# Kernel tuning notes

Hardware: AMD Instinct MI355X
Metric: run time of the kernel (lower is better)

Reference implementation:

```python
import jax, jax.numpy as jnp
import numpy as np


def _conv2d(x, w, b):
    # x: [B,C,H,W], w: [O,I,kh,kw] (SAME padding, stride 1)
    y = jax.lax.conv_general_dilated(x, w, (1, 1), 'SAME',
                                     dimension_numbers=('NCHW', 'OIHW', 'NCHW'))
    return y + b[None, :, None, None]


def _conv1x1(x, w, b):
    # w: [O,C], b: [O]
    return jnp.einsum('oc,bchw->bohw', w, x) + b[None, :, None, None]


def _attention(xq, xkv, w, b):
    # w: [3,C,C] (q,k,v), b: [3,C]. Tokens = spatial positions, features = channels.
    B, C, H, W = xq.shape
    q = _conv1x1(xq, w[0], b[0]).reshape(B, C, H * W).transpose(0, 2, 1)   # [B,HW,C]
    k = _conv1x1(xkv, w[1], b[1]).reshape(B, C, H * W).transpose(0, 2, 1)
    v = _conv1x1(xkv, w[2], b[2]).reshape(B, C, H * W).transpose(0, 2, 1)
    scale = 1.0 / jnp.sqrt(jnp.asarray(C, xq.dtype))  # d_k = channels
    a = jax.nn.softmax(jnp.einsum('bnc,bmc->bnm', q, k) * scale, axis=-1)  # [B,HW,HW]
    out = jnp.einsum('bnm,bmc->bnc', a, v).transpose(0, 2, 1).reshape(B, C, H, W)
    return out + xq


def _cell(x, h, c, w, b):
    gates = _conv2d(jnp.concatenate([x, h], axis=1), w, b)
    i, f, o, g = jnp.split(gates, 4, axis=1)
    i, f, o, g = jax.nn.sigmoid(i), jax.nn.sigmoid(f), jax.nn.sigmoid(o), jnp.tanh(g)
    c_new = f * c + i * g
    h_new = o * jnp.tanh(c_new)
    return h_new, c_new


def setup_inputs() -> dict:
    key = jax.random.key(0)
    ks = iter(jax.random.split(key, 32))
    B, T, Cin, H, W = 2, 3, 1, 32, 32
    HID, L, K, OUT = 64, 2, 3, 1
    s = 0.02
    d = {
        'x1_seq': jax.random.normal(next(ks), (B, T, Cin, H, W), jnp.float32),
        'x2_seq': jax.random.normal(next(ks), (B, T, Cin, H, W), jnp.float32),
        # ConvLSTM gate convs: layer0 in = Cin+HID, layer1 in = 2*HID, per stream
        'conv1_w0': jax.random.normal(next(ks), (4 * HID, Cin + HID, K, K)) * s,
        'conv1_b0': jnp.zeros((4 * HID,)),
        'conv1_w1': jax.random.normal(next(ks), (4 * HID, 2 * HID, K, K)) * s,
        'conv1_b1': jnp.zeros((4 * HID,)),
        'conv2_w0': jax.random.normal(next(ks), (4 * HID, Cin + HID, K, K)) * s,
        'conv2_b0': jnp.zeros((4 * HID,)),
        'conv2_w1': jax.random.normal(next(ks), (4 * HID, 2 * HID, K, K)) * s,
        'conv2_b1': jnp.zeros((4 * HID,)),
        # attention 1x1 convs, stacked [L, 3(q/k/v), HID, HID]
        'sah_w': jax.random.normal(next(ks), (L, 3, HID, HID)) * s,
        'sah_b': jnp.zeros((L, 3, HID)),
        'sac_w': jax.random.normal(next(ks), (L, 3, HID, HID)) * s,
        'sac_b': jnp.zeros((L, 3, HID)),
        'cah_w': jax.random.normal(next(ks), (L, 3, HID, HID)) * s,
        'cah_b': jnp.zeros((L, 3, HID)),
        'cac_w': jax.random.normal(next(ks), (L, 3, HID, HID)) * s,
        'cac_b': jnp.zeros((L, 3, HID)),
        # decoder
        'dec_w1': jax.random.normal(next(ks), (HID, HID, 3, 3)) * s,
        'dec_b1': jnp.zeros((HID,)),
        'dec_w2': jax.random.normal(next(ks), (OUT, HID, 3, 3)) * s,
        'dec_b2': jnp.zeros((OUT,)),
        'future_steps': 4,
    }
    return d


def reference(x1_seq, x2_seq,
              conv1_w0, conv1_b0, conv1_w1, conv1_b1,
              conv2_w0, conv2_b0, conv2_w1, conv2_b1,
              sah_w, sah_b, sac_w, sac_b, cah_w, cah_b, cac_w, cac_b,
              dec_w1, dec_b1, dec_w2, dec_b2, future_steps):
    B, T, _, H, W = x1_seq.shape
    HID = sah_w.shape[-1]
    L = sah_w.shape[0]
    cw1 = [(conv1_w0, conv1_b0), (conv1_w1, conv1_b1)]
    cw2 = [(conv2_w0, conv2_b0), (conv2_w1, conv2_b1)]

    def decoder(h):
        return _conv2d(jax.nn.relu(_conv2d(h, dec_w1, dec_b1)), dec_w2, dec_b2)

    z = jnp.zeros((B, HID, H, W), x1_seq.dtype)
    h1s, c1s = [z] * L, [z] * L
    h2s, c2s = [z] * L, [z] * L

    def step(x1_t, x2_t, h1s, c1s, h2s, c2s):
        h1s, c1s, h2s, c2s = list(h1s), list(c1s), list(h2s), list(c2s)
        for l in range(L):
            h1, c1 = _cell(x1_t, h1s[l], c1s[l], *cw1[l])
            h2, c2 = _cell(x2_t, h2s[l], c2s[l], *cw2[l])
            h1 = _attention(h1, h1, sah_w[l], sah_b[l])
            c1 = _attention(c1, c1, sac_w[l], sac_b[l])
            h2 = _attention(h2, h2, sah_w[l], sah_b[l])
            c2 = _attention(c2, c2, sac_w[l], sac_b[l])
            tag_h1, tag_c1 = h1, c1
            h1 = _attention(h1, h2, cah_w[l], cah_b[l])
            c1 = _attention(c1, c2, cac_w[l], cac_b[l])
            h2 = _attention(h2, tag_h1, cah_w[l], cah_b[l])
            c2 = _attention(c2, tag_c1, cac_w[l], cac_b[l])
            h1s[l], c1s[l], h2s[l], c2s[l] = h1, c1, h2, c2
            x1_t, x2_t = h1, h2
        return h1s, c1s, h2s, c2s

    warm1, warm2 = [], []
    for t in range(T):
        h1s, c1s, h2s, c2s = step(x1_seq[:, t], x2_seq[:, t], h1s, c1s, h2s, c2s)
        if t < T - 1:
            warm1.append(h1s[-1])
            warm2.append(h2s[-1])
    pred_warm1 = jnp.stack([decoder(h) for h in warm1], axis=1)
    pred_warm2 = jnp.stack([decoder(h) for h in warm2], axis=1)

    preds1, preds2 = [], []
    for _ in range(int(future_steps)):
        p1 = decoder(h1s[-1])
        p2 = decoder(h2s[-1])
        preds1.append(p1)
        preds2.append(p2)
        h1s, c1s, h2s, c2s = step(p1, p2, h1s, c1s, h2s, c2s)
    preds1 = jnp.stack(preds1, axis=1)
    preds2 = jnp.stack(preds2, axis=1)
    return preds1, preds2, pred_warm1, pred_warm2
```

## Files before the change

kernel.cpp:

```cpp
#include <hip/hip_runtime.h>
#include <math.h>

#define BB 2
#define HIDC 64
#define HWN 1024

struct CellArgs {
  const float* x[2]; long xbs;
  const float* h[2]; const float* c[2];
  const float* w[2]; const float* bias[2];
  float* ho[2]; float* co[2];
};

template<int CX>
__global__ __launch_bounds__(512) void cell_kernel(CellArgs a) {
  constexpr int CT = CX + HIDC;
  constexpr int CH = (CT + 1) / 2;
  __shared__ float sIn[CT * 48];
  __shared__ float sGa[256 * 17];
  __shared__ float sGb[256 * 17];
  const int tile = blockIdx.x;
  const int b = blockIdx.y;
  const int st = blockIdx.z;
  const int ty0 = (tile >> 3) << 2, tx0 = (tile & 7) << 2;
  const float* xp = a.x[st] + (size_t)b * a.xbs;
  const float* hp = a.h[st] + (size_t)b * HIDC * HWN;

  for (int idx = threadIdx.x; idx < CT * 36; idx += 512) {
    int ic = idx / 36, pos = idx - ic * 36;
    int iy = pos / 6, ix = pos - iy * 6;
    int gy = ty0 - 1 + iy, gx = tx0 - 1 + ix;
    float v = 0.f;
    if ((unsigned)gy < 32u && (unsigned)gx < 32u) {
      v = (ic < CX) ? xp[ic * HWN + gy * 32 + gx]
                    : hp[(ic - CX) * HWN + gy * 32 + gx];
    }
    sIn[ic * 48 + iy * 8 + ix] = v;
  }
  __syncthreads();

  const int oc = threadIdx.x & 255;
  const int hh = threadIdx.x >> 8;
  const int icb = hh ? CH : 0, ice = hh ? CT : CH;
  float acc[16];
#pragma unroll
  for (int p = 0; p < 16; ++p) acc[p] = 0.f;
  const float* wp = a.w[st] + (size_t)oc * CT * 9;
  for (int ic = icb; ic < ice; ++ic) {
    float w9[9];
#pragma unroll
    for (int t = 0; t < 9; ++t) w9[t] = wp[ic * 9 + t];
    float in[36];
#pragma unroll
    for (int iy = 0; iy < 6; ++iy) {
      float4 v4 = *(const float4*)&sIn[ic * 48 + iy * 8];
      float2 v2 = *(const float2*)&sIn[ic * 48 + iy * 8 + 4];
      in[iy * 6 + 0] = v4.x; in[iy * 6 + 1] = v4.y; in[iy * 6 + 2] = v4.z;
      in[iy * 6 + 3] = v4.w; in[iy * 6 + 4] = v2.x; in[iy * 6 + 5] = v2.y;
    }
#pragma unroll
    for (int ky = 0; ky < 3; ++ky)
#pragma unroll
      for (int kx = 0; kx < 3; ++kx) {
        const float wv = w9[ky * 3 + kx];
#pragma unroll
        for (int py = 0; py < 4; ++py)
#pragma unroll
          for (int px = 0; px < 4; ++px)
            acc[py * 4 + px] += wv * in[(py + ky) * 6 + (px + kx)];
      }
  }
  float* sGh = hh ? sGb : sGa;
#pragma unroll
  for (int p = 0; p < 16; ++p) sGh[oc * 17 + p] = acc[p];
  __syncthreads();

  const float* cp = a.c[st] + (size_t)b * HIDC * HWN;
  float* hop = a.ho[st] + (size_t)b * HIDC * HWN;
  float* cop = a.co[st] + (size_t)b * HIDC * HWN;
  const float* bias = a.bias[st];
  for (int idx = threadIdx.x; idx < HIDC * 16; idx += 512) {
    int hc = idx >> 4, p = idx & 15;
    float gi = sGa[hc * 17 + p]         + sGb[hc * 17 + p]         + bias[hc];
    float gf = sGa[(hc + 64) * 17 + p]  + sGb[(hc + 64) * 17 + p]  + bias[hc + 64];
    float go = sGa[(hc + 128) * 17 + p] + sGb[(hc + 128) * 17 + p] + bias[hc + 128];
    float gg = sGa[(hc + 192) * 17 + p] + sGb[(hc + 192) * 17 + p] + bias[hc + 192];
    gi = 1.f / (1.f + expf(-gi));
    gf = 1.f / (1.f + expf(-gf));
    go = 1.f / (1.f + expf(-go));
    gg = tanhf(gg);
    int off = hc * HWN + (ty0 + (p >> 2)) * 32 + tx0 + (p & 3);
    float cn = gf * cp[off] + gi * gg;
    cop[off] = cn;
    hop[off] = go * tanhf(cn);
  }
}

struct QkvArgs {
  const float* xq[4]; const float* xkv[4];
  const float* w[4]; const float* bias[4];
  float* Q; float* K; float* V;
};

__global__ __launch_bounds__(256) void qkv_kernel(QkvArgs a) {
  __shared__ float sWt[64 * 68];
  const int ptile = blockIdx.x, b = blockIdx.y;
  const int attn = blockIdx.z / 3, proj = blockIdx.z % 3;
  const float* x = (proj == 0 ? a.xq[attn] : a.xkv[attn]) + (size_t)b * HIDC * HWN;
  const float* w = a.w[attn] + proj * 64 * 64;
  const float* bias = a.bias[attn] + proj * 64;
  float* dst = (proj == 0 ? a.Q : (proj == 1 ? a.K : a.V)) +
               ((size_t)attn * BB + b) * HWN * HIDC;
  for (int i = threadIdx.x; i < 4096; i += 256) {
    int o = i >> 6, c = i & 63;
    sWt[c * 68 + o] = w[i];
  }
  __syncthreads();
  const int og = threadIdx.x & 3, pq = threadIdx.x >> 2;
  const int p0 = ptile * 128 + pq * 2;
  float acc[2][16];
#pragma unroll
  for (int k = 0; k < 16; ++k) {
    float bv = bias[og * 16 + k];
    acc[0][k] = bv; acc[1][k] = bv;
  }
  for (int c = 0; c < 64; ++c) {
    float2 xv = *(const float2*)&x[c * HWN + p0];
#pragma unroll
    for (int k = 0; k < 16; k += 4) {
      float4 wv = *(const float4*)&sWt[c * 68 + og * 16 + k];
      acc[0][k+0] += xv.x*wv.x; acc[0][k+1] += xv.x*wv.y; acc[0][k+2] += xv.x*wv.z; acc[0][k+3] += xv.x*wv.w;
      acc[1][k+0] += xv.y*wv.x; acc[1][k+1] += xv.y*wv.y; acc[1][k+2] += xv.y*wv.z; acc[1][k+3] += xv.y*wv.w;
    }
  }
#pragma unroll
  for (int px = 0; px < 2; ++px) {
    float* d = dst + (size_t)(p0 + px) * HIDC + og * 16;
#pragma unroll
    for (int k = 0; k < 16; k += 4) {
      float4 v; v.x = acc[px][k]; v.y = acc[px][k+1]; v.z = acc[px][k+2]; v.w = acc[px][k+3];
      *(float4*)&d[k] = v;
    }
  }
}

struct AttnPArgs { const float* Q; const float* K; const float* V; float* pbuf; };

__global__ __launch_bounds__(256) void attn_part(AttnPArgs a) {
  __shared__ float sQt[64 * 36];
  __shared__ float sKt[64 * 68];
  __shared__ float sV [64 * 68];
  __shared__ float sPt[64 * 36];
  const int qt = blockIdx.x >> 2, ks = blockIdx.x & 3;
  const int b = blockIdx.y, at = blockIdx.z;
  const size_t base = ((size_t)at * BB + b) * HWN * HIDC;
  const float* Qp = a.Q + base + (size_t)qt * 32 * HIDC;
  const float* Kp = a.K + base;
  const float* Vp = a.V + base;
  const int tid = threadIdx.x;
  {
    int r = tid >> 3, c0 = (tid & 7) * 8;
    const float* q = Qp + r * HIDC + c0;
#pragma unroll
    for (int k = 0; k < 8; k += 4) {
      float4 v = *(const float4*)&q[k];
      sQt[(c0 + k + 0) * 36 + r] = v.x * 0.125f;
      sQt[(c0 + k + 1) * 36 + r] = v.y * 0.125f;
      sQt[(c0 + k + 2) * 36 + r] = v.z * 0.125f;
      sQt[(c0 + k + 3) * 36 + r] = v.w * 0.125f;
    }
  }
  const int tc = tid & 15, tr = tid >> 4;
  const int r0 = tr * 2, j0 = tc * 4;
  const int kj = tid & 63, kch = (tid >> 6) * 16;
  const int sj = tid >> 2, scs = (tid & 3) * 16;
  float m0 = -1e30f, m1 = -1e30f, l0 = 0.f, l1 = 0.f;
  float o00=0,o01=0,o02=0,o03=0,o10=0,o11=0,o12=0,o13=0;

  const int ktb = ks * 4;
  float4 kr[4], vr[4];
  {
    const float* kp = Kp + (size_t)(ktb * 64 + kj) * HIDC + kch;
    const float* vp = Vp + (size_t)(ktb * 64 + sj) * HIDC + scs;
#pragma unroll
    for (int q = 0; q < 4; ++q) {
      kr[q] = *(const float4*)&kp[q * 4];
      vr[q] = *(const float4*)&vp[q * 4];
    }
  }

  for (int kk = 0; kk < 4; ++kk) {
    __syncthreads();
#pragma unroll
    for (int q = 0; q < 4; ++q) {
      sKt[(kch + q * 4 + 0) * 68 + kj] = kr[q].x;
      sKt[(kch + q * 4 + 1) * 68 + kj] = kr[q].y;
      sKt[(kch + q * 4 + 2) * 68 + kj] = kr[q].z;
      sKt[(kch + q * 4 + 3) * 68 + kj] = kr[q].w;
      *(float4*)&sV[sj * 68 + scs + q * 4] = vr[q];
    }
    __syncthreads();
    if (kk < 3) {
      const float* kp = Kp + (size_t)((ktb + kk + 1) * 64 + kj) * HIDC + kch;
      const float* vp = Vp + (size_t)((ktb + kk + 1) * 64 + sj) * HIDC + scs;
#pragma unroll
      for (int q = 0; q < 4; ++q) {
        kr[q] = *(const float4*)&kp[q * 4];
        vr[q] = *(const float4*)&vp[q * 4];
      }
    }
    float s00=0,s01=0,s02=0,s03=0,s10=0,s11=0,s12=0,s13=0;
#pragma unroll 4
    for (int c = 0; c < 64; ++c) {
      float2 qv = *(const float2*)&sQt[c * 36 + r0];
      float4 kv = *(const float4*)&sKt[c * 68 + j0];
      s00 += qv.x*kv.x; s01 += qv.x*kv.y; s02 += qv.x*kv.z; s03 += qv.x*kv.w;
      s10 += qv.y*kv.x; s11 += qv.y*kv.y; s12 += qv.y*kv.z; s13 += qv.y*kv.w;
    }
    float mt0 = fmaxf(fmaxf(s00, s01), fmaxf(s02, s03));
    float mt1 = fmaxf(fmaxf(s10, s11), fmaxf(s12, s13));
#pragma unroll
    for (int d = 1; d < 16; d <<= 1) {
      mt0 = fmaxf(mt0, __shfl_xor(mt0, d));
      mt1 = fmaxf(mt1, __shfl_xor(mt1, d));
    }
    float mn0 = fmaxf(m0, mt0), mn1 = fmaxf(m1, mt1);
    float al0 = __expf(m0 - mn0), al1 = __expf(m1 - mn1);
    s00 = __expf(s00 - mn0); s01 = __expf(s01 - mn0);
    s02 = __expf(s02 - mn0); s03 = __expf(s03 - mn0);
    s10 = __expf(s10 - mn1); s11 = __expf(s11 - mn1);
    s12 = __expf(s12 - mn1); s13 = __expf(s13 - mn1);
    float ps0 = s00 + s01 + s02 + s03, ps1 = s10 + s11 + s12 + s13;
#pragma unroll
    for (int d = 1; d < 16; d <<= 1) {
      ps0 += __shfl_xor(ps0, d);
      ps1 += __shfl_xor(ps1, d);
    }
    l0 = l0 * al0 + ps0; l1 = l1 * al1 + ps1;
    m0 = mn0; m1 = mn1;
    o00*=al0; o01*=al0; o02*=al0; o03*=al0;
    o10*=al1; o11*=al1; o12*=al1; o13*=al1;
    float2 pv;
    pv.x=s00; pv.y=s10; *(float2*)&sPt[(j0+0)*36 + r0] = pv;
    pv.x=s01; pv.y=s11; *(float2*)&sPt[(j0+1)*36 + r0] = pv;
    pv.x=s02; pv.y=s12; *(float2*)&sPt[(j0+2)*36 + r0] = pv;
    pv.x=s03; pv.y=s13; *(float2*)&sPt[(j0+3)*36 + r0] = pv;
    __syncthreads();
#pragma unroll 4
    for (int j = 0; j < 64; ++j) {
      float2 pj = *(const float2*)&sPt[j * 36 + r0];
      float4 vv = *(const float4*)&sV[j * 68 + j0];
      o00 += pj.x*vv.x; o01 += pj.x*vv.y; o02 += pj.x*vv.z; o03 += pj.x*vv.w;
      o10 += pj.y*vv.x; o11 += pj.y*vv.y; o12 += pj.y*vv.z; o13 += pj.y*vv.w;
    }
  }
  float* pb = a.pbuf + ((((size_t)at * BB + b) * 32 + qt) * 4 + ks) * 2112;
  float4 w0; w0.x=o00; w0.y=o01; w0.z=o02; w0.w=o03;
  float4 w1; w1.x=o10; w1.y=o11; w1.z=o12; w1.w=o13;
  *(float4*)&pb[r0 * 64 + j0] = w0;
  *(float4*)&pb[(r0 + 1) * 64 + j0] = w1;
  if (tc == 0) {
    pb[2048 + r0] = m0; pb[2048 + r0 + 1] = m1;
    pb[2080 + r0] = l0; pb[2080 + r0 + 1] = l1;
  }
}

struct AttnMArgs { const float* pbuf; const float* xq[4]; float* out[4]; };

__global__ __launch_bounds__(256) void attn_merge(AttnMArgs a) {
  const int qt = blockIdx.x, b = blockIdx.y, at = blockIdx.z;
  const float* pb = a.pbuf + (((size_t)at * BB + b) * 32 + qt) * 4 * 2112;
  const int c = threadIdx.x >> 2;
  const int rq = (threadIdx.x & 3) * 8;
  const float* xq = a.xq[at] + (size_t)b * HIDC * HWN;
  float* op = a.out[at] + (size_t)b * HIDC * HWN;
  const int p0 = qt * 32 + rq;
  float res[8];
#pragma unroll
  for (int rr = 0; rr < 8; ++rr) {
    int r = rq + rr;
    float mm0 = pb[2048 + r],            mm1 = pb[2112 + 2048 + r];
    float mm2 = pb[2*2112 + 2048 + r],   mm3 = pb[3*2112 + 2048 + r];
    float M = fmaxf(fmaxf(mm0, mm1), fmaxf(mm2, mm3));
    float w0 = __expf(mm0 - M), w1 = __expf(mm1 - M);
    float w2 = __expf(mm2 - M), w3 = __expf(mm3 - M);
    float L = pb[2080 + r]*w0 + pb[2112 + 2080 + r]*w1 +
              pb[2*2112 + 2080 + r]*w2 + pb[3*2112 + 2080 + r]*w3;
    float acc = pb[r*64 + c]*w0 + pb[2112 + r*64 + c]*w1 +
                pb[2*2112 + r*64 + c]*w2 + pb[3*2112 + r*64 + c]*w3;
    res[rr] = acc / L;
  }
  float4 x0 = *(const float4*)&xq[(size_t)c * HWN + p0];
  float4 x1 = *(const float4*)&xq[(size_t)c * HWN + p0 + 4];
  float4 o0, o1;
  o0.x = res[0] + x0.x; o0.y = res[1] + x0.y; o0.z = res[2] + x0.z; o0.w = res[3] + x0.w;
  o1.x = res[4] + x1.x; o1.y = res[5] + x1.y; o1.z = res[6] + x1.z; o1.w = res[7] + x1.w;
  *(float4*)&op[(size_t)c * HWN + p0] = o0;
  *(float4*)&op[(size_t)c * HWN + p0 + 4] = o1;
}

struct Dec1Args { const float* in[2]; const float* w; const float* b; float* tmp; };

__global__ __launch_bounds__(512) void dec1_kernel(Dec1Args a) {
  __shared__ float sIn[64 * 48];
  __shared__ float sHa[64 * 17];
  __shared__ float sHb[64 * 17];
  const int tile = blockIdx.x, b = blockIdx.y, st = blockIdx.z;
  const int ty0 = (tile >> 3) << 2, tx0 = (tile & 7) << 2;
  const float* ip = a.in[st] + (size_t)b * HIDC * HWN;
  for (int idx = threadIdx.x; idx < 64 * 36; idx += 512) {
    int ic = idx / 36, pos = idx - ic * 36;
    int iy = pos / 6, ix = pos - iy * 6;
    int gy = ty0 - 1 + iy, gx = tx0 - 1 + ix;
    float v = 0.f;
    if ((unsigned)gy < 32u && (unsigned)gx < 32u) v = ip[ic * HWN + gy * 32 + gx];
    sIn[ic * 48 + iy * 8 + ix] = v;
  }
  __syncthreads();
  const int oc = threadIdx.x & 63, ps = (threadIdx.x >> 6) & 3;
  const int hh = threadIdx.x >> 8;
  const int icb = hh * 32, ice = icb + 32;
  float acc0 = 0.f, acc1 = 0.f, acc2 = 0.f, acc3 = 0.f;
  const float* wp = a.w + (size_t)oc * 64 * 9;
  for (int ic = icb; ic < ice; ++ic) {
    float in[18];
#pragma unroll
    for (int ry = 0; ry < 3; ++ry) {
      float4 v4 = *(const float4*)&sIn[ic * 48 + (ps + ry) * 8];
      float2 v2 = *(const float2*)&sIn[ic * 48 + (ps + ry) * 8 + 4];
      in[ry*6+0]=v4.x; in[ry*6+1]=v4.y; in[ry*6+2]=v4.z; in[ry*6+3]=v4.w;
      in[ry*6+4]=v2.x; in[ry*6+5]=v2.y;
    }
#pragma unroll
    for (int ky = 0; ky < 3; ++ky)
#pragma unroll
      for (int kx = 0; kx < 3; ++kx) {
        float wv = wp[ic * 9 + ky * 3 + kx];
        acc0 += wv * in[ky * 6 + kx + 0];
        acc1 += wv * in[ky * 6 + kx + 1];
        acc2 += wv * in[ky * 6 + kx + 2];
        acc3 += wv * in[ky * 6 + kx + 3];
      }
  }
  float* sH = hh ? sHb : sHa;
  sH[oc * 17 + ps * 4 + 0] = acc0;
  sH[oc * 17 + ps * 4 + 1] = acc1;
  sH[oc * 17 + ps * 4 + 2] = acc2;
  sH[oc * 17 + ps * 4 + 3] = acc3;
  __syncthreads();
  float* dst = a.tmp + ((size_t)st * BB + b) * HIDC * HWN;
  for (int idx = threadIdx.x; idx < 1024; idx += 512) {
    int oc2 = idx >> 4, p = idx & 15;
    float v = sHa[oc2 * 17 + p] + sHb[oc2 * 17 + p] + a.b[oc2];
    v = fmaxf(v, 0.f);
    dst[(size_t)oc2 * HWN + (ty0 + (p >> 2)) * 32 + tx0 + (p & 3)] = v;
  }
}

struct Dec2Args { const float* tmp; const float* w; const float* b;
                  float* dst0; float* dst1; long bstr; };

__global__ __launch_bounds__(256) void dec2_kernel(Dec2Args a) {
  __shared__ float sIn[64 * 48];
  __shared__ float sW[64 * 9];
  const int tile = blockIdx.x, b = blockIdx.y, st = blockIdx.z;
  const int ty0 = (tile >> 3) << 2, tx0 = (tile & 7) << 2;
  const float* ip = a.tmp + ((size_t)st * BB + b) * HIDC * HWN;
  for (int idx = threadIdx.x; idx < 64 * 36; idx += 256) {
    int ic = idx / 36, pos = idx - ic * 36;
    int iy = pos / 6, ix = pos - iy * 6;
    int gy = ty0 - 1 + iy, gx = tx0 - 1 + ix;
    float v = 0.f;
    if ((unsigned)gy < 32u && (unsigned)gx < 32u) v = ip[ic * HWN + gy * 32 + gx];
    sIn[ic * 48 + iy * 8 + ix] = v;
  }
  for (int idx = threadIdx.x; idx < 576; idx += 256) sW[idx] = a.w[idx];
  __syncthreads();
  const int px = threadIdx.x >> 4, icg = threadIdx.x & 15;
  const int py = px >> 2, pxx = px & 3;
  float acc = 0.f;
#pragma unroll
  for (int i = 0; i < 4; ++i) {
    int ic = icg * 4 + i;
    const float* row = &sIn[ic * 48];
    const float* wv = &sW[ic * 9];
#pragma unroll
    for (int ky = 0; ky < 3; ++ky)
#pragma unroll
      for (int kx = 0; kx < 3; ++kx)
        acc += wv[ky * 3 + kx] * row[(py + ky) * 8 + pxx + kx];
  }
#pragma unroll
  for (int d = 1; d < 16; d <<= 1) acc += __shfl_xor(acc, d);
  if (icg == 0) {
    float* d = (st == 0 ? a.dst0 : a.dst1);
    d[(size_t)b * a.bstr + (ty0 + py) * 32 + tx0 + pxx] = acc + a.b[0];
  }
}

extern "C" void kernel_launch(void* const* d_in, const int* in_sizes, int n_in,
                              void* d_out, int out_size, void* d_ws, size_t ws_size,
                              hipStream_t stream) {
  (void)in_sizes; (void)n_in; (void)out_size; (void)ws_size;
  const float* x1_seq = (const float*)d_in[0];
  const float* x2_seq = (const float*)d_in[1];
  const float* c1w[2] = {(const float*)d_in[2], (const float*)d_in[4]};
  const float* c1b[2] = {(const float*)d_in[3], (const float*)d_in[5]};
  const float* c2w[2] = {(const float*)d_in[6], (const float*)d_in[8]};
  const float* c2b[2] = {(const float*)d_in[7], (const float*)d_in[9]};
  const float* sah_w = (const float*)d_in[10]; const float* sah_b = (const float*)d_in[11];
  const float* sac_w = (const float*)d_in[12]; const float* sac_b = (const float*)d_in[13];
  const float* cah_w = (const float*)d_in[14]; const float* cah_b = (const float*)d_in[15];
  const float* cac_w = (const float*)d_in[16]; const float* cac_b = (const float*)d_in[17];
  const float* dw1 = (const float*)d_in[18]; const float* db1 = (const float*)d_in[19];
  const float* dw2 = (const float*)d_in[20]; const float* db2 = (const float*)d_in[21];
  float* out = (float*)d_out;
  float* ws = (float*)d_ws;

  const size_t SPL = (size_t)BB * HIDC * HWN;
  float* h1s = ws;
  float* c1s = h1s + 2 * SPL;
  float* h2s = c1s + 2 * SPL;
  float* c2s = h2s + 2 * SPL;
  float* hc1 = c2s + 2 * SPL;
  float* cc1 = hc1 + SPL;
  float* hc2 = cc1 + SPL;
  float* cc2 = hc2 + SPL;
  float* hs1 = cc2 + SPL;
  float* cs1 = hs1 + SPL;
  float* hs2 = cs1 + SPL;
  float* cs2 = hs2 + SPL;
  float* Qb  = cs2 + SPL;
  float* Kb  = Qb + 4 * SPL;
  float* Vb  = Kb + 4 * SPL;
  float* dtmp = Vb + 4 * SPL;
  float* pbuf = dtmp + 2 * SPL;

  hipMemsetAsync(ws, 0, 8 * SPL * sizeof(float), stream);

  const dim3 blk(256);
  const dim3 blk2(512);

  auto attn_stage = [&](const float* q0, const float* q1, const float* q2, const float* q3,
                        const float* k0, const float* k1, const float* k2, const float* k3,
                        const float* wh, const float* bh, const float* wc, const float* bc,
                        float* o0, float* o1, float* o2, float* o3) {
    QkvArgs qa;
    qa.xq[0]=q0; qa.xq[1]=q1; qa.xq[2]=q2; qa.xq[3]=q3;
    qa.xkv[0]=k0; qa.xkv[1]=k1; qa.xkv[2]=k2; qa.xkv[3]=k3;
    qa.w[0]=wh; qa.w[1]=wc; qa.w[2]=wh; qa.w[3]=wc;
    qa.bias[0]=bh; qa.bias[1]=bc; qa.bias[2]=bh; qa.bias[3]=bc;
    qa.Q=Qb; qa.K=Kb; qa.V=Vb;
    qkv_kernel<<<dim3(8, BB, 12), blk, 0, stream>>>(qa);
    AttnPArgs ap; ap.Q=Qb; ap.K=Kb; ap.V=Vb; ap.pbuf=pbuf;
    attn_part<<<dim3(128, BB, 4), blk, 0, stream>>>(ap);
    AttnMArgs am; am.pbuf=pbuf;
    am.xq[0]=q0; am.xq[1]=q1; am.xq[2]=q2; am.xq[3]=q3;
    am.out[0]=o0; am.out[1]=o1; am.out[2]=o2; am.out[3]=o3;
    attn_merge<<<dim3(32, BB, 4), blk, 0, stream>>>(am);
  };

  auto decode = [&](long off1, long off2, long bstr) {
    Dec1Args d1; d1.in[0] = h1s + SPL; d1.in[1] = h2s + SPL;
    d1.w = dw1; d1.b = db1; d1.tmp = dtmp;
    dec1_kernel<<<dim3(64, BB, 2), blk2, 0, stream>>>(d1);
    Dec2Args d2; d2.tmp = dtmp; d2.w = dw2; d2.b = db2;
    d2.dst0 = out + off1; d2.dst1 = out + off2; d2.bstr = bstr;
    dec2_kernel<<<dim3(64, BB, 2), blk, 0, stream>>>(d2);
  };

  for (int s = 0; s < 6; ++s) {
    const float *x1, *x2; long xbs;
    if (s < 3) { x1 = x1_seq + s * HWN; x2 = x2_seq + s * HWN; xbs = 3 * HWN; }
    else       { x1 = out + (s - 3) * HWN; x2 = out + 8192 + (s - 3) * HWN; xbs = 4 * HWN; }

    for (int l = 0; l < 2; ++l) {
      if (l == 1) { x1 = h1s; x2 = h2s; xbs = (long)HIDC * HWN; }
      CellArgs ca;
      ca.x[0] = x1; ca.x[1] = x2; ca.xbs = xbs;
      ca.h[0] = h1s + l * SPL; ca.h[1] = h2s + l * SPL;
      ca.c[0] = c1s + l * SPL; ca.c[1] = c2s + l * SPL;
      ca.w[0] = c1w[l]; ca.w[1] = c2w[l];
      ca.bias[0] = c1b[l]; ca.bias[1] = c2b[l];
      ca.ho[0] = hc1; ca.ho[1] = hc2; ca.co[0] = cc1; ca.co[1] = cc2;
      if (l == 0) cell_kernel<1><<<dim3(64, BB, 2), blk2, 0, stream>>>(ca);
      else        cell_kernel<64><<<dim3(64, BB, 2), blk2, 0, stream>>>(ca);

      attn_stage(hc1, cc1, hc2, cc2,
                 hc1, cc1, hc2, cc2,
                 sah_w + l * 12288, sah_b + l * 192,
                 sac_w + l * 12288, sac_b + l * 192,
                 hs1, cs1, hs2, cs2);
      attn_stage(hs1, cs1, hs2, cs2,
                 hs2, cs2, hs1, cs1,
                 cah_w + l * 12288, cah_b + l * 192,
                 cac_w + l * 12288, cac_b + l * 192,
                 h1s + l * SPL, c1s + l * SPL, h2s + l * SPL, c2s + l * SPL);
    }

    if (s == 0)      decode(16384,        20480,        2048);
    else if (s == 1) decode(16384 + 1024, 20480 + 1024, 2048);
    else             decode((s - 2) * HWN, 8192 + (s - 2) * HWN, 4096);
  }
}
```

Measured before the change: 2.588 ms.

## Transpose conv weights for coalesced loads and enlarge attention query tiles

A new kernel transposes the ConvLSTM gate and decoder conv weights once per call so that threads reading different output channels hit consecutive addresses. This replaces strided per-thread weight loads with coalesced ones. The attention partial kernel moves from 32-query to 64-query tiles with a 4x4 register tile per thread and XOR-swizzled shared memory, and the merge kernel caches the softmax rescale weights in shared memory. The qkv kernel now computes one pixel per thread. The cost is an extra transpose launch and workspace, fewer attention blocks, and higher register pressure.

```diff
diff --git a/kernel.cpp b/kernel.cpp
--- a/kernel.cpp
+++ b/kernel.cpp
@@ -4,6 +4,21 @@
 #define BB 2
 #define HIDC 64
 #define HWN 1024
+
+struct TWArgs { const float* src[5]; float* dst[5]; int icn9[5]; int osh[5]; };
+
+__global__ __launch_bounds__(256) void transpose_w(TWArgs a) {
+  const int arr = blockIdx.y;
+  const int icn9 = a.icn9[arr], osh = a.osh[arr];
+  const int ocn = 1 << osh;
+  const float* s = a.src[arr];
+  float* d = a.dst[arr];
+  const int n = icn9 << osh;
+  for (int i = blockIdx.x * 256 + threadIdx.x; i < n; i += gridDim.x * 256) {
+    int oc = i & (ocn - 1), tt = i >> osh;
+    d[i] = s[(size_t)oc * icn9 + tt];
+  }
+}
 
 struct CellArgs {
   const float* x[2]; long xbs;
@@ -45,11 +60,11 @@
   float acc[16];
 #pragma unroll
   for (int p = 0; p < 16; ++p) acc[p] = 0.f;
-  const float* wp = a.w[st] + (size_t)oc * CT * 9;
+  const float* wp = a.w[st];
   for (int ic = icb; ic < ice; ++ic) {
     float w9[9];
 #pragma unroll
-    for (int t = 0; t < 9; ++t) w9[t] = wp[ic * 9 + t];
+    for (int t = 0; t < 9; ++t) w9[t] = wp[(ic * 9 + t) * 256 + oc];
     float in[36];
 #pragma unroll
     for (int iy = 0; iy < 6; ++iy) {
@@ -116,187 +131,211 @@
     sWt[c * 68 + o] = w[i];
   }
   __syncthreads();
-  const int og = threadIdx.x & 3, pq = threadIdx.x >> 2;
-  const int p0 = ptile * 128 + pq * 2;
-  float acc[2][16];
-#pragma unroll
-  for (int k = 0; k < 16; ++k) {
-    float bv = bias[og * 16 + k];
-    acc[0][k] = bv; acc[1][k] = bv;
-  }
+  const int pq = threadIdx.x & 63, og = threadIdx.x >> 6;
+  const int p0 = ptile * 64 + pq;
+  float acc[16];
+#pragma unroll
+  for (int k = 0; k < 16; ++k) acc[k] = bias[og * 16 + k];
   for (int c = 0; c < 64; ++c) {
-    float2 xv = *(const float2*)&x[c * HWN + p0];
+    float xv = x[c * HWN + p0];
 #pragma unroll
     for (int k = 0; k < 16; k += 4) {
       float4 wv = *(const float4*)&sWt[c * 68 + og * 16 + k];
-      acc[0][k+0] += xv.x*wv.x; acc[0][k+1] += xv.x*wv.y; acc[0][k+2] += xv.x*wv.z; acc[0][k+3] += xv.x*wv.w;
-      acc[1][k+0] += xv.y*wv.x; acc[1][k+1] += xv.y*wv.y; acc[1][k+2] += xv.y*wv.z; acc[1][k+3] += xv.y*wv.w;
-    }
-  }
-#pragma unroll
-  for (int px = 0; px < 2; ++px) {
-    float* d = dst + (size_t)(p0 + px) * HIDC + og * 16;
-#pragma unroll
-    for (int k = 0; k < 16; k += 4) {
-      float4 v; v.x = acc[px][k]; v.y = acc[px][k+1]; v.z = acc[px][k+2]; v.w = acc[px][k+3];
-      *(float4*)&d[k] = v;
-    }
+      acc[k+0] += xv * wv.x; acc[k+1] += xv * wv.y;
+      acc[k+2] += xv * wv.z; acc[k+3] += xv * wv.w;
+    }
+  }
+  float* d = dst + (size_t)p0 * HIDC + og * 16;
+#pragma unroll
+  for (int k = 0; k < 16; k += 4) {
+    float4 v; v.x = acc[k]; v.y = acc[k+1]; v.z = acc[k+2]; v.w = acc[k+3];
+    *(float4*)&d[k] = v;
   }
 }
 
 struct AttnPArgs { const float* Q; const float* K; const float* V; float* pbuf; };
 
 __global__ __launch_bounds__(256) void attn_part(AttnPArgs a) {
-  __shared__ float sQt[64 * 36];
-  __shared__ float sKt[64 * 68];
-  __shared__ float sV [64 * 68];
-  __shared__ float sPt[64 * 36];
+  __shared__ float sQt[64 * 64];
+  __shared__ float sKt[64 * 64];
+  __shared__ float sV [64 * 64];
+  __shared__ float sPt[64 * 64];
   const int qt = blockIdx.x >> 2, ks = blockIdx.x & 3;
   const int b = blockIdx.y, at = blockIdx.z;
   const size_t base = ((size_t)at * BB + b) * HWN * HIDC;
-  const float* Qp = a.Q + base + (size_t)qt * 32 * HIDC;
+  const float* Qp = a.Q + base + (size_t)qt * 64 * HIDC;
   const float* Kp = a.K + base;
   const float* Vp = a.V + base;
   const int tid = threadIdx.x;
   {
-    int r = tid >> 3, c0 = (tid & 7) * 8;
-    const float* q = Qp + r * HIDC + c0;
-#pragma unroll
-    for (int k = 0; k < 8; k += 4) {
+    const int qr = tid & 63, qc0 = (tid >> 6) * 16;
+    const float* q = Qp + qr * HIDC + qc0;
+#pragma unroll
+    for (int k = 0; k < 16; k += 4) {
       float4 v = *(const float4*)&q[k];
-      sQt[(c0 + k + 0) * 36 + r] = v.x * 0.125f;
-      sQt[(c0 + k + 1) * 36 + r] = v.y * 0.125f;
-      sQt[(c0 + k + 2) * 36 + r] = v.z * 0.125f;
-      sQt[(c0 + k + 3) * 36 + r] = v.w * 0.125f;
+      sQt[(qc0 + k + 0) * 64 + qr] = v.x * 0.125f;
+      sQt[(qc0 + k + 1) * 64 + qr] = v.y * 0.125f;
+      sQt[(qc0 + k + 2) * 64 + qr] = v.z * 0.125f;
+      sQt[(qc0 + k + 3) * 64 + qr] = v.w * 0.125f;
     }
   }
   const int tc = tid & 15, tr = tid >> 4;
-  const int r0 = tr * 2, j0 = tc * 4;
+  const int j0 = tc * 4, r0 = tr * 4;
   const int kj = tid & 63, kch = (tid >> 6) * 16;
-  const int sj = tid >> 2, scs = (tid & 3) * 16;
-  float m0 = -1e30f, m1 = -1e30f, l0 = 0.f, l1 = 0.f;
-  float o00=0,o01=0,o02=0,o03=0,o10=0,o11=0,o12=0,o13=0;
+  const int vj = tid >> 2, vc0 = (tid & 3) * 16;
+  float m[4], l[4], o[4][4];
+#pragma unroll
+  for (int i = 0; i < 4; ++i) {
+    m[i] = -1e30f; l[i] = 0.f;
+    o[i][0] = 0; o[i][1] = 0; o[i][2] = 0; o[i][3] = 0;
+  }
 
   const int ktb = ks * 4;
   float4 kr[4], vr[4];
   {
     const float* kp = Kp + (size_t)(ktb * 64 + kj) * HIDC + kch;
-    const float* vp = Vp + (size_t)(ktb * 64 + sj) * HIDC + scs;
-#pragma unroll
-    for (int q = 0; q < 4; ++q) {
-      kr[q] = *(const float4*)&kp[q * 4];
-      vr[q] = *(const float4*)&vp[q * 4];
+    const float* vp = Vp + (size_t)(ktb * 64 + vj) * HIDC + vc0;
+#pragma unroll
+    for (int q2 = 0; q2 < 4; ++q2) {
+      kr[q2] = *(const float4*)&kp[q2 * 4];
+      vr[q2] = *(const float4*)&vp[q2 * 4];
     }
   }
 
   for (int kk = 0; kk < 4; ++kk) {
     __syncthreads();
 #pragma unroll
-    for (int q = 0; q < 4; ++q) {
-      sKt[(kch + q * 4 + 0) * 68 + kj] = kr[q].x;
-      sKt[(kch + q * 4 + 1) * 68 + kj] = kr[q].y;
-      sKt[(kch + q * 4 + 2) * 68 + kj] = kr[q].z;
-      sKt[(kch + q * 4 + 3) * 68 + kj] = kr[q].w;
-      *(float4*)&sV[sj * 68 + scs + q * 4] = vr[q];
+    for (int q2 = 0; q2 < 4; ++q2) {
+      sKt[(kch + q2 * 4 + 0) * 64 + kj] = kr[q2].x;
+      sKt[(kch + q2 * 4 + 1) * 64 + kj] = kr[q2].y;
+      sKt[(kch + q2 * 4 + 2) * 64 + kj] = kr[q2].z;
+      sKt[(kch + q2 * 4 + 3) * 64 + kj] = kr[q2].w;
+      int c = vc0 + q2 * 4;
+      *(float4*)&sV[vj * 64 + (c ^ ((vj & 7) * 4))] = vr[q2];
     }
     __syncthreads();
     if (kk < 3) {
       const float* kp = Kp + (size_t)((ktb + kk + 1) * 64 + kj) * HIDC + kch;
-      const float* vp = Vp + (size_t)((ktb + kk + 1) * 64 + sj) * HIDC + scs;
-#pragma unroll
-      for (int q = 0; q < 4; ++q) {
-        kr[q] = *(const float4*)&kp[q * 4];
-        vr[q] = *(const float4*)&vp[q * 4];
+      const float* vp = Vp + (size_t)((ktb + kk + 1) * 64 + vj) * HIDC + vc0;
+#pragma unroll
+      for (int q2 = 0; q2 < 4; ++q2) {
+        kr[q2] = *(const float4*)&kp[q2 * 4];
+        vr[q2] = *(const float4*)&vp[q2 * 4];
       }
     }
-    float s00=0,s01=0,s02=0,s03=0,s10=0,s11=0,s12=0,s13=0;
+    float s[4][4];
+#pragma unroll
+    for (int i = 0; i < 4; ++i) { s[i][0]=0; s[i][1]=0; s[i][2]=0; s[i][3]=0; }
 #pragma unroll 4
     for (int c = 0; c < 64; ++c) {
-      float2 qv = *(const float2*)&sQt[c * 36 + r0];
-      float4 kv = *(const float4*)&sKt[c * 68 + j0];
-      s00 += qv.x*kv.x; s01 += qv.x*kv.y; s02 += qv.x*kv.z; s03 += qv.x*kv.w;
-      s10 += qv.y*kv.x; s11 += qv.y*kv.y; s12 += qv.y*kv.z; s13 += qv.y*kv.w;
-    }
-    float mt0 = fmaxf(fmaxf(s00, s01), fmaxf(s02, s03));
-    float mt1 = fmaxf(fmaxf(s10, s11), fmaxf(s12, s13));
+      float4 q4 = *(const float4*)&sQt[c * 64 + r0];
+      float4 k4 = *(const float4*)&sKt[c * 64 + j0];
+      s[0][0]+=q4.x*k4.x; s[0][1]+=q4.x*k4.y; s[0][2]+=q4.x*k4.z; s[0][3]+=q4.x*k4.w;
+      s[1][0]+=q4.y*k4.x; s[1][1]+=q4.y*k4.y; s[1][2]+=q4.y*k4.z; s[1][3]+=q4.y*k4.w;
+      s[2][0]+=q4.z*k4.x; s[2][1]+=q4.z*k4.y; s[2][2]+=q4.z*k4.z; s[2][3]+=q4.z*k4.w;
+      s[3][0]+=q4.w*k4.x; s[3][1]+=q4.w*k4.y; s[3][2]+=q4.w*k4.z; s[3][3]+=q4.w*k4.w;
+    }
+    float mt[4];
+#pragma unroll
+    for (int i = 0; i < 4; ++i)
+      mt[i] = fmaxf(fmaxf(s[i][0], s[i][1]), fmaxf(s[i][2], s[i][3]));
 #pragma unroll
     for (int d = 1; d < 16; d <<= 1) {
-      mt0 = fmaxf(mt0, __shfl_xor(mt0, d));
-      mt1 = fmaxf(mt1, __shfl_xor(mt1, d));
-    }
-    float mn0 = fmaxf(m0, mt0), mn1 = fmaxf(m1, mt1);
-    float al0 = __expf(m0 - mn0), al1 = __expf(m1 - mn1);
-    s00 = __expf(s00 - mn0); s01 = __expf(s01 - mn0);
-    s02 = __expf(s02 - mn0); s03 = __expf(s03 - mn0);
-    s10 = __expf(s10 - mn1); s11 = __expf(s11 - mn1);
-    s12 = __expf(s12 - mn1); s13 = __expf(s13 - mn1);
-    float ps0 = s00 + s01 + s02 + s03, ps1 = s10 + s11 + s12 + s13;
+#pragma unroll
+      for (int i = 0; i < 4; ++i) mt[i] = fmaxf(mt[i], __shfl_xor(mt[i], d));
+    }
+    float al[4];
+#pragma unroll
+    for (int i = 0; i < 4; ++i) {
+      float mn = fmaxf(m[i], mt[i]);
+      al[i] = __expf(m[i] - mn);
+      m[i] = mn;
+      s[i][0] = __expf(s[i][0] - mn); s[i][1] = __expf(s[i][1] - mn);
+      s[i][2] = __expf(s[i][2] - mn); s[i][3] = __expf(s[i][3] - mn);
+    }
+    float ps[4];
+#pragma unroll
+    for (int i = 0; i < 4; ++i) ps[i] = s[i][0] + s[i][1] + s[i][2] + s[i][3];
 #pragma unroll
     for (int d = 1; d < 16; d <<= 1) {
-      ps0 += __shfl_xor(ps0, d);
-      ps1 += __shfl_xor(ps1, d);
-    }
-    l0 = l0 * al0 + ps0; l1 = l1 * al1 + ps1;
-    m0 = mn0; m1 = mn1;
-    o00*=al0; o01*=al0; o02*=al0; o03*=al0;
-    o10*=al1; o11*=al1; o12*=al1; o13*=al1;
-    float2 pv;
-    pv.x=s00; pv.y=s10; *(float2*)&sPt[(j0+0)*36 + r0] = pv;
-    pv.x=s01; pv.y=s11; *(float2*)&sPt[(j0+1)*36 + r0] = pv;
-    pv.x=s02; pv.y=s12; *(float2*)&sPt[(j0+2)*36 + r0] = pv;
-    pv.x=s03; pv.y=s13; *(float2*)&sPt[(j0+3)*36 + r0] = pv;
+#pragma unroll
+      for (int i = 0; i < 4; ++i) ps[i] += __shfl_xor(ps[i], d);
+    }
+#pragma unroll
+    for (int i = 0; i < 4; ++i) {
+      l[i] = l[i] * al[i] + ps[i];
+      o[i][0] *= al[i]; o[i][1] *= al[i]; o[i][2] *= al[i]; o[i][3] *= al[i];
+    }
+#pragma unroll
+    for (int jj = 0; jj < 4; ++jj) {
+      int j = j0 + jj;
+      float4 pv; pv.x = s[0][jj]; pv.y = s[1][jj]; pv.z = s[2][jj]; pv.w = s[3][jj];
+      *(float4*)&sPt[j * 64 + (r0 ^ ((j & 7) * 4))] = pv;
+    }
     __syncthreads();
 #pragma unroll 4
     for (int j = 0; j < 64; ++j) {
-      float2 pj = *(const float2*)&sPt[j * 36 + r0];
-      float4 vv = *(const float4*)&sV[j * 68 + j0];
-      o00 += pj.x*vv.x; o01 += pj.x*vv.y; o02 += pj.x*vv.z; o03 += pj.x*vv.w;
-      o10 += pj.y*vv.x; o11 += pj.y*vv.y; o12 += pj.y*vv.z; o13 += pj.y*vv.w;
-    }
-  }
-  float* pb = a.pbuf + ((((size_t)at * BB + b) * 32 + qt) * 4 + ks) * 2112;
-  float4 w0; w0.x=o00; w0.y=o01; w0.z=o02; w0.w=o03;
-  float4 w1; w1.x=o10; w1.y=o11; w1.z=o12; w1.w=o13;
-  *(float4*)&pb[r0 * 64 + j0] = w0;
-  *(float4*)&pb[(r0 + 1) * 64 + j0] = w1;
+      float4 p4 = *(const float4*)&sPt[j * 64 + (r0 ^ ((j & 7) * 4))];
+      float4 v4 = *(const float4*)&sV [j * 64 + (j0 ^ ((j & 7) * 4))];
+      o[0][0]+=p4.x*v4.x; o[0][1]+=p4.x*v4.y; o[0][2]+=p4.x*v4.z; o[0][3]+=p4.x*v4.w;
+      o[1][0]+=p4.y*v4.x; o[1][1]+=p4.y*v4.y; o[1][2]+=p4.y*v4.z; o[1][3]+=p4.y*v4.w;
+      o[2][0]+=p4.z*v4.x; o[2][1]+=p4.z*v4.y; o[2][2]+=p4.z*v4.z; o[2][3]+=p4.z*v4.w;
+      o[3][0]+=p4.w*v4.x; o[3][1]+=p4.w*v4.y; o[3][2]+=p4.w*v4.z; o[3][3]+=p4.w*v4.w;
+    }
+  }
+  float* pb = a.pbuf + ((((size_t)at * BB + b) * 16 + qt) * 4 + ks) * 4224;
+#pragma unroll
+  for (int i = 0; i < 4; ++i) {
+    float4 w; w.x = o[i][0]; w.y = o[i][1]; w.z = o[i][2]; w.w = o[i][3];
+    *(float4*)&pb[(r0 + i) * 64 + j0] = w;
+  }
   if (tc == 0) {
-    pb[2048 + r0] = m0; pb[2048 + r0 + 1] = m1;
-    pb[2080 + r0] = l0; pb[2080 + r0 + 1] = l1;
+#pragma unroll
+    for (int i = 0; i < 4; ++i) {
+      pb[4096 + r0 + i] = m[i];
+      pb[4160 + r0 + i] = l[i];
+    }
   }
 }
 
 struct AttnMArgs { const float* pbuf; const float* xq[4]; float* out[4]; };
 
 __global__ __launch_bounds__(256) void attn_merge(AttnMArgs a) {
+  __shared__ float sW[4][64];
+  __shared__ float sL[64];
   const int qt = blockIdx.x, b = blockIdx.y, at = blockIdx.z;
-  const float* pb = a.pbuf + (((size_t)at * BB + b) * 32 + qt) * 4 * 2112;
-  const int c = threadIdx.x >> 2;
-  const int rq = (threadIdx.x & 3) * 8;
+  const float* pb = a.pbuf + (((size_t)at * BB + b) * 16 + qt) * 4 * 4224;
+  if (threadIdx.x < 64) {
+    int r = threadIdx.x;
+    float m0 = pb[4096 + r],          m1 = pb[4224 + 4096 + r];
+    float m2 = pb[2*4224 + 4096 + r], m3 = pb[3*4224 + 4096 + r];
+    float M = fmaxf(fmaxf(m0, m1), fmaxf(m2, m3));
+    float w0 = __expf(m0 - M), w1 = __expf(m1 - M);
+    float w2 = __expf(m2 - M), w3 = __expf(m3 - M);
+    sW[0][r] = w0; sW[1][r] = w1; sW[2][r] = w2; sW[3][r] = w3;
+    sL[r] = pb[4160 + r] * w0 + pb[4224 + 4160 + r] * w1 +
+            pb[2*4224 + 4160 + r] * w2 + pb[3*4224 + 4160 + r] * w3;
+  }
+  __syncthreads();
+  const int c = threadIdx.x >> 2, rg = (threadIdx.x & 3) * 16;
   const float* xq = a.xq[at] + (size_t)b * HIDC * HWN;
   float* op = a.out[at] + (size_t)b * HIDC * HWN;
-  const int p0 = qt * 32 + rq;
-  float res[8];
-#pragma unroll
-  for (int rr = 0; rr < 8; ++rr) {
-    int r = rq + rr;
-    float mm0 = pb[2048 + r],            mm1 = pb[2112 + 2048 + r];
-    float mm2 = pb[2*2112 + 2048 + r],   mm3 = pb[3*2112 + 2048 + r];
-    float M = fmaxf(fmaxf(mm0, mm1), fmaxf(mm2, mm3));
-    float w0 = __expf(mm0 - M), w1 = __expf(mm1 - M);
-    float w2 = __expf(mm2 - M), w3 = __expf(mm3 - M);
-    float L = pb[2080 + r]*w0 + pb[2112 + 2080 + r]*w1 +
-              pb[2*2112 + 2080 + r]*w2 + pb[3*2112 + 2080 + r]*w3;
-    float acc = pb[r*64 + c]*w0 + pb[2112 + r*64 + c]*w1 +
-                pb[2*2112 + r*64 + c]*w2 + pb[3*2112 + r*64 + c]*w3;
-    res[rr] = acc / L;
-  }
-  float4 x0 = *(const float4*)&xq[(size_t)c * HWN + p0];
-  float4 x1 = *(const float4*)&xq[(size_t)c * HWN + p0 + 4];
-  float4 o0, o1;
-  o0.x = res[0] + x0.x; o0.y = res[1] + x0.y; o0.z = res[2] + x0.z; o0.w = res[3] + x0.w;
-  o1.x = res[4] + x1.x; o1.y = res[5] + x1.y; o1.z = res[6] + x1.z; o1.w = res[7] + x1.w;
-  *(float4*)&op[(size_t)c * HWN + p0] = o0;
-  *(float4*)&op[(size_t)c * HWN + p0 + 4] = o1;
+  const int p0 = qt * 64 + rg;
+#pragma unroll
+  for (int rr4 = 0; rr4 < 16; rr4 += 4) {
+    float rv[4];
+#pragma unroll
+    for (int k = 0; k < 4; ++k) {
+      int r = rg + rr4 + k;
+      float acc = pb[r*64 + c] * sW[0][r] + pb[4224 + r*64 + c] * sW[1][r]
+                + pb[2*4224 + r*64 + c] * sW[2][r] + pb[3*4224 + r*64 + c] * sW[3][r];
+      rv[k] = acc / sL[r];
+    }
+    float4 x4 = *(const float4*)&xq[(size_t)c * HWN + p0 + rr4];
+    float4 res; res.x = rv[0] + x4.x; res.y = rv[1] + x4.y;
+    res.z = rv[2] + x4.z; res.w = rv[3] + x4.w;
+    *(float4*)&op[(size_t)c * HWN + p0 + rr4] = res;
+  }
 }
 
 struct Dec1Args { const float* in[2]; const float* w; const float* b; float* tmp; };
@@ -321,8 +360,11 @@
   const int hh = threadIdx.x >> 8;
   const int icb = hh * 32, ice = icb + 32;
   float acc0 = 0.f, acc1 = 0.f, acc2 = 0.f, acc3 = 0.f;
-  const float* wp = a.w + (size_t)oc * 64 * 9;
+  const float* wp = a.w;
   for (int ic = icb; ic < ice; ++ic) {
+    float w9[9];
+#pragma unroll
+    for (int t = 0; t < 9; ++t) w9[t] = wp[(ic * 9 + t) * 64 + oc];
     float in[18];
 #pragma unroll
     for (int ry = 0; ry < 3; ++ry) {
@@ -335,7 +377,7 @@
     for (int ky = 0; ky < 3; ++ky)
 #pragma unroll
       for (int kx = 0; kx < 3; ++kx) {
-        float wv = wp[ic * 9 + ky * 3 + kx];
+        float wv = w9[ky * 3 + kx];
         acc0 += wv * in[ky * 6 + kx + 0];
         acc1 += wv * in[ky * 6 + kx + 1];
         acc2 += wv * in[ky * 6 + kx + 2];
@@ -435,11 +477,26 @@
   float* Vb  = Kb + 4 * SPL;
   float* dtmp = Vb + 4 * SPL;
   float* pbuf = dtmp + 2 * SPL;
+  float* wt10 = pbuf + (size_t)4 * BB * 16 * 4 * 4224;
+  float* wt11 = wt10 + 585 * 256;
+  float* wt20 = wt11 + 1152 * 256;
+  float* wt21 = wt20 + 585 * 256;
+  float* wtd  = wt21 + 1152 * 256;
 
   hipMemsetAsync(ws, 0, 8 * SPL * sizeof(float), stream);
 
   const dim3 blk(256);
   const dim3 blk2(512);
+
+  {
+    TWArgs tw;
+    tw.src[0] = c1w[0]; tw.dst[0] = wt10; tw.icn9[0] = 585;  tw.osh[0] = 8;
+    tw.src[1] = c1w[1]; tw.dst[1] = wt11; tw.icn9[1] = 1152; tw.osh[1] = 8;
+    tw.src[2] = c2w[0]; tw.dst[2] = wt20; tw.icn9[2] = 585;  tw.osh[2] = 8;
+    tw.src[3] = c2w[1]; tw.dst[3] = wt21; tw.icn9[3] = 1152; tw.osh[3] = 8;
+    tw.src[4] = dw1;    tw.dst[4] = wtd;  tw.icn9[4] = 576;  tw.osh[4] = 6;
+    transpose_w<<<dim3(32, 5), blk, 0, stream>>>(tw);
+  }
 
   auto attn_stage = [&](const float* q0, const float* q1, const float* q2, const float* q3,
                         const float* k0, const float* k1, const float* k2, const float* k3,
@@ -451,18 +508,18 @@
     qa.w[0]=wh; qa.w[1]=wc; qa.w[2]=wh; qa.w[3]=wc;
     qa.bias[0]=bh; qa.bias[1]=bc; qa.bias[2]=bh; qa.bias[3]=bc;
     qa.Q=Qb; qa.K=Kb; qa.V=Vb;
-    qkv_kernel<<<dim3(8, BB, 12), blk, 0, stream>>>(qa);
+    qkv_kernel<<<dim3(16, BB, 12), blk, 0, stream>>>(qa);
     AttnPArgs ap; ap.Q=Qb; ap.K=Kb; ap.V=Vb; ap.pbuf=pbuf;
-    attn_part<<<dim3(128, BB, 4), blk, 0, stream>>>(ap);
+    attn_part<<<dim3(64, BB, 4), blk, 0, stream>>>(ap);
     AttnMArgs am; am.pbuf=pbuf;
     am.xq[0]=q0; am.xq[1]=q1; am.xq[2]=q2; am.xq[3]=q3;
     am.out[0]=o0; am.out[1]=o1; am.out[2]=o2; am.out[3]=o3;
-    attn_merge<<<dim3(32, BB, 4), blk, 0, stream>>>(am);
+    attn_merge<<<dim3(16, BB, 4), blk, 0, stream>>>(am);
   };
 
   auto decode = [&](long off1, long off2, long bstr) {
     Dec1Args d1; d1.in[0] = h1s + SPL; d1.in[1] = h2s + SPL;
-    d1.w = dw1; d1.b = db1; d1.tmp = dtmp;
+    d1.w = wtd; d1.b = db1; d1.tmp = dtmp;
     dec1_kernel<<<dim3(64, BB, 2), blk2, 0, stream>>>(d1);
     Dec2Args d2; d2.tmp = dtmp; d2.w = dw2; d2.b = db2;
     d2.dst0 = out + off1; d2.dst1 = out + off2; d2.bstr = bstr;
@@ -480,7 +537,8 @@
       ca.x[0] = x1; ca.x[1] = x2; ca.xbs = xbs;
       ca.h[0] = h1s + l * SPL; ca.h[1] = h2s + l * SPL;
       ca.c[0] = c1s + l * SPL; ca.c[1] = c2s + l * SPL;
-      ca.w[0] = c1w[l]; ca.w[1] = c2w[l];
+      ca.w[0] = (l == 0) ? wt10 : wt11;
+      ca.w[1] = (l == 0) ? wt20 : wt21;
       ca.bias[0] = c1b[l]; ca.bias[1] = c2b[l];
       ca.ho[0] = hc1; ca.ho[1] = hc2; ca.co[0] = cc1; ca.co[1] = cc2;
       if (l == 0) cell_kernel<1><<<dim3(64, BB, 2), blk2, 0, stream>>>(ca);
```

New measurement: 2.432 ms. 1.06x faster.
